# Kernel tuning notes

Hardware: AMD Instinct MI355X
Metric: run time of the kernel (lower is better)

The kernel has to match this reference:

```python
import jax, jax.numpy as jnp
import numpy as np

B, E, H, DEPTH = 4096, 512, 512, 1
STRIDE = 2 * H * (DEPTH + 1)      # 2048
DEPTH_SIZE = 2 * 4 * H            # 4096


def setup_inputs() -> dict:
    key = jax.random.key(0)
    ks = jax.random.split(key, 12)
    s = 0.02
    return {
        "X": jax.random.normal(ks[0], (B, E), jnp.float32),
        "prev_a": jax.random.normal(ks[1], (B, DEPTH + 1, H), jnp.float32),
        "prev_b": jax.random.normal(ks[2], (B, DEPTH + 1, H), jnp.float32),
        "prev_depth": jax.random.randint(ks[3], (B, 1), 0, DEPTH + 1, jnp.int32),
        "Wa00": jax.random.normal(ks[4], (H, E + 2 * H), jnp.float32) * s,
        "Wa10": jax.random.normal(ks[5], (H, E + H), jnp.float32) * s,
        "Wb00": jax.random.normal(ks[6], (H, E + 2 * H), jnp.float32) * s,
        "Wb11": jax.random.normal(ks[7], (H, E + H), jnp.float32) * s,
        "Wb10": jax.random.normal(ks[8], (H, E + H), jnp.float32) * s,
        "Wb01": jax.random.normal(ks[9], (H, E + 2 * H), jnp.float32) * s,
        "Watt": jax.random.normal(ks[10], (4, DEPTH_SIZE * DEPTH), jnp.float32) * s,
    }


def reference(X, prev_a, prev_b, prev_depth, Wa00, Wa10, Wb00, Wb11, Wb10, Wb01, Watt):
    b = X.shape[0]
    pd = prev_depth.astype(X.dtype)  # [B,1], broadcasts over feature dim
    zeros2h = jnp.zeros((b, 2 * H), X.dtype)
    ab00, ab01, ab10, ab11 = [zeros2h], [zeros2h], [zeros2h], [zeros2h]
    for d in range(1, DEPTH + 1):
        fd = jnp.float32(d)
        a_d, a_dm1 = prev_a[:, d, :], prev_a[:, d - 1, :]
        b_d, b_dm1 = prev_b[:, d, :], prev_b[:, d - 1, :]
        # 'lt' branch multiplies zeros -> drop it; keep eq/gt terms only
        eq0, gt0 = (pd == fd).astype(X.dtype), (pd > fd).astype(X.dtype)
        eqp, gtp = (pd + 1 == fd).astype(X.dtype), (pd + 1 > fd).astype(X.dtype)
        eqm, gtm = (pd - 1 == fd).astype(X.dtype), (pd - 1 > fd).astype(X.dtype)
        fork_join_a = a_d
        nofork_nojoin_a = jnp.concatenate((X, b_dm1, a_d), 1) @ Wa00.T
        fork_nojoin_a = jnp.concatenate((X, b_dm1), 1) @ Wa10.T
        nofork_join_a = a_dm1
        na00 = eq0 * nofork_nojoin_a + gt0 * a_d
        na11 = eq0 * fork_join_a + gt0 * a_d
        na10 = eqp * fork_nojoin_a + gtp * a_d
        na01 = eqm * nofork_join_a + gtm * a_d
        fork_join_b = jnp.concatenate((X, b_d), 1) @ Wb11.T
        nofork_nojoin_b = jnp.concatenate((X, a_d, na00), 1) @ Wb00.T
        fork_nojoin_b = jnp.concatenate((X, na10), 1) @ Wb10.T
        nofork_join_b = jnp.concatenate((X, b_dm1, a_d), 1) @ Wb01.T
        nb00 = eq0 * nofork_nojoin_b + gt0 * b_d
        nb11 = eq0 * fork_join_b + gt0 * b_d
        nb10 = eqp * fork_nojoin_b + gtp * b_d
        nb01 = eqm * nofork_join_b + gtm * b_d
        ab00.append(jnp.concatenate((na00, nb00), 1))
        ab01.append(jnp.concatenate((na01, nb01), 1))
        ab10.append(jnp.concatenate((na10, nb10), 1))
        ab11.append(jnp.concatenate((na11, nb11), 1))
    # each branch: stack over depth+1 -> [B, stride]; concat branches -> [B, 4*stride]
    flats = [jnp.stack(lst, 1).reshape(b, -1) for lst in (ab00, ab01, ab10, ab11)]
    ns = jnp.concatenate(flats, 1)  # [B, 4*STRIDE]
    att = jax.nn.softmax(ns[:, DEPTH_SIZE:] @ Watt.T, axis=-1)  # [B,4]
    e0 = (pd == 0).astype(X.dtype)
    ed = (pd == DEPTH).astype(X.dtype)
    mask = jnp.concatenate((1 - e0, 1 - e0, 1 - ed, 1 - e0), 1)  # [B,4]
    att_vars = mask * att
    # np tiny underflows to 0 in fp32 -> selection is one-hot at the row max
    sel = jnp.sign(att_vars - att_vars.max(1, keepdims=True)) + 1.0
    # striper/stripe_expander bmm == per-row selection of one stride-block
    hidden = jnp.einsum('bc,bcs->bs', sel, ns.reshape(b, 4, STRIDE))
    hidden = hidden.reshape(b, DEPTH + 1, 2 * H)
    next_a = hidden[:, :, :H]
    next_b = hidden[:, :, H:]
    sel_i = sel.astype(prev_depth.dtype)
    pd0 = prev_depth[:, 0]
    next_depth = (sel_i[:, 0] * pd0 + sel_i[:, 1] * (pd0 - 1)
                  + sel_i[:, 2] * (pd0 + 1) + sel_i[:, 3] * pd0)[:, None]
    f = (sel[:, 2] + sel[:, 3])[:, None]
    j = (sel[:, 1] + sel[:, 3])[:, None]
    return next_a, next_b, next_depth, (f, j)
```

## Files before the change

kernel.cpp:

```cpp
#include <hip/hip_runtime.h>
#include <hip/hip_bf16.h>
#include <stdint.h>


typedef __attribute__((ext_vector_type(8))) short bf16x8;
typedef __attribute__((ext_vector_type(4))) float f32x4;

#define MB_ ((size_t)1 << 20)

static __device__ __forceinline__ unsigned short f2bf(float x) {
  unsigned u = __float_as_uint(x);
  return (unsigned short)((u + 0x7FFFu + ((u >> 16) & 1u)) >> 16);
}
static __device__ __forceinline__ float bf2f(unsigned short b) {
  return __uint_as_float((unsigned)b << 16);
}
static __device__ __forceinline__ void cvt8(float4 v0, float4 v1, uint4& hi, uint4& lo) {
  float v[8] = {v0.x, v0.y, v0.z, v0.w, v1.x, v1.y, v1.z, v1.w};
  unsigned hw[4], lw[4];
#pragma unroll
  for (int j = 0; j < 4; ++j) {
    unsigned short h0 = f2bf(v[2 * j]), h1 = f2bf(v[2 * j + 1]);
    unsigned short l0 = f2bf(v[2 * j] - bf2f(h0));
    unsigned short l1 = f2bf(v[2 * j + 1] - bf2f(h1));
    hw[j] = (unsigned)h0 | ((unsigned)h1 << 16);
    lw[j] = (unsigned)l0 | ((unsigned)l1 << 16);
  }
  hi = make_uint4(hw[0], hw[1], hw[2], hw[3]);
  lo = make_uint4(lw[0], lw[1], lw[2], lw[3]);
}

__global__ void kinit(float* nextA, float* nextB, int* cnt, int Bn) {
  long i = (long)blockIdx.x * blockDim.x + threadIdx.x;
  long st = (long)gridDim.x * blockDim.x;
  long n4 = (long)Bn * 128;
  float4 z = make_float4(0.f, 0.f, 0.f, 0.f);
  for (long t = i; t < n4; t += st) {
    long row = t >> 7;
    int off = (int)(t & 127);
    ((float4*)(nextA + row * 1024))[off] = z;
    ((float4*)(nextB + row * 1024))[off] = z;
  }
  if (blockIdx.x == 0 && threadIdx.x < 16) cnt[threadIdx.x] = 0;
}

struct CvtSeg { const float* src; unsigned short* dst; int srcStride; int gprow; long gbase; };
struct CvtArgs { CvtSeg s[5]; long total; };

__global__ void kcvt(CvtArgs a) {
  long g0 = (long)blockIdx.x * blockDim.x + threadIdx.x;
  long st = (long)gridDim.x * blockDim.x;
  for (long g = g0; g < a.total; g += st) {
    const float* src = a.s[0].src;
    unsigned short* dst = a.s[0].dst;
    int stride = a.s[0].srcStride, gp = a.s[0].gprow;
    long base = 0;
#pragma unroll
    for (int t = 1; t < 5; ++t) {
      if (g >= a.s[t].gbase) {
        src = a.s[t].src; dst = a.s[t].dst;
        stride = a.s[t].srcStride; gp = a.s[t].gprow; base = a.s[t].gbase;
      }
    }
    long lg = g - base;
    int row = (int)(lg / gp);
    int kp = (int)(lg - (long)row * gp);
    const float* p = src + (long)row * stride + kp * 8;
    uint4 hi, lo;
    cvt8(*(const float4*)p, *(const float4*)(p + 4), hi, lo);
    unsigned short* d = dst + (long)row * ((long)gp * 16) + (long)(kp >> 2) * 64 + (kp & 3) * 8;
    *(uint4*)d = hi;
    *(uint4*)(d + 32) = lo;
  }
}

__global__ void kclassify(const int* __restrict__ pdep, float* dep, float* fo, float* jo,
                          int* cnt, int* list0, int* list1, int Bn) {
  int r = blockIdx.x * blockDim.x + threadIdx.x;
  if (r >= Bn) return;
  if (pdep[r] == 0) {
    int p = atomicAdd(&cnt[0], 1);
    list0[p] = r;
    dep[r] = 1.0f; fo[r] = 1.0f; jo[r] = 0.0f;
  } else {
    int p = atomicAdd(&cnt[1], 1);
    list1[p] = r;
  }
}

struct GArgs {
  const float *X, *pa, *pb;
  float *nb11ws, *na00ws, *na10ws;
  const unsigned short *Wa10p, *Wb10p, *Wb11p, *Wa00p, *Wb00p;
  float *nextA, *nextB;
  const int *cnt, *list0, *list1, *list2, *list2i;
};

__global__ __launch_bounds__(256, 4) void gemm_mfma(GArgs G, int modeBase, int bpm) {
  int mode = (int)blockIdx.x / bpm + modeBase;
  int bl = (int)blockIdx.x % bpm;
  int xcd = bl & 7, g = bl >> 3;
  int nt = g & 7, mt = (g >> 3) * 8 + xcd;

  const int* lst; int cntv, ksteps;
  const unsigned short* W;
  if (mode == 0)      { lst = G.list0; cntv = G.cnt[0]; ksteps = 32; W = G.Wa10p; }
  else if (mode == 1) { lst = G.list1; cntv = G.cnt[1]; ksteps = 32; W = G.Wb11p; }
  else if (mode == 2) { lst = G.list1; cntv = G.cnt[1]; ksteps = 48; W = G.Wa00p; }
  else if (mode == 3) { lst = G.list0; cntv = G.cnt[0]; ksteps = 32; W = G.Wb10p; }
  else                { lst = G.list2; cntv = G.cnt[2]; ksteps = 48; W = G.Wb00p; }
  if (mt * 64 >= cntv) return;

  const int tid = threadIdx.x;
  const int arow = tid >> 2, kg = tid & 3;
  int mg = mt * 64 + arow;
  if (mg > cntv - 1) mg = cntv - 1;
  int r01 = lst[mg];
  const float* ab0 = G.X + (long)r01 * 512 + kg * 8;
  const float* ab1;
  const float* ab2 = nullptr;
  if (mode == 0)      ab1 = G.pb + (long)r01 * 1024 + kg * 8;
  else if (mode == 1) ab1 = G.pb + (long)r01 * 1024 + 512 + kg * 8;
  else if (mode == 2) {
    ab1 = G.pb + (long)r01 * 1024 + kg * 8;
    ab2 = G.pa + (long)r01 * 1024 + 512 + kg * 8;
  } else if (mode == 3) {
    ab1 = G.na10ws + (long)mg * 512 + kg * 8;
  } else {
    ab1 = G.pa + (long)r01 * 1024 + 512 + kg * 8;
    ab2 = G.na00ws + (long)G.list2i[mg] * 512 + kg * 8;
  }
  long wb = (long)(nt * 64 + arow) * (long)(ksteps * 64) + kg * 8;

  __shared__ unsigned short lds[2][2][4096];

  float4 av0, av1;
  uint4 bhr, blr;
  auto gload = [&](int kb) {
    const float* p = (kb < 16) ? ab0 : (kb < 32) ? ab1 : ab2;
    p += (kb & 15) * 32;
    av0 = *(const float4*)p;
    av1 = *(const float4*)(p + 4);
    const unsigned short* q = W + wb + (long)kb * 64;
    bhr = *(const uint4*)q;
    blr = *(const uint4*)(q + 32);
  };
  auto lstore = [&](int b) {
    uint4 hi, lo;
    cvt8(av0, av1, hi, lo);
    *(uint4*)&lds[b][0][((kg) * 64 + arow) * 8] = hi;
    *(uint4*)&lds[b][0][((kg + 4) * 64 + arow) * 8] = lo;
    *(uint4*)&lds[b][1][((kg) * 64 + arow) * 8] = bhr;
    *(uint4*)&lds[b][1][((kg + 4) * 64 + arow) * 8] = blr;
  };

  const int w = tid >> 6, lane = tid & 63;
  const int wrow = (w >> 1) * 32, wcol = (w & 1) * 32;
  const int gq = lane >> 4, lr = lane & 15;

  f32x4 acc[2][2];
#pragma unroll
  for (int i = 0; i < 2; ++i)
#pragma unroll
    for (int j = 0; j < 2; ++j) acc[i][j] = (f32x4){0.f, 0.f, 0.f, 0.f};

  gload(0);
  lstore(0);
  __syncthreads();
  int cur = 0;
  for (int kb = 0; kb < ksteps; ++kb) {
    bf16x8 ah[2], al[2], bh[2], bl[2];
#pragma unroll
    for (int t = 0; t < 2; ++t) {
      ah[t] = *(const bf16x8*)&lds[cur][0][(gq * 64 + wrow + t * 16 + lr) * 8];
      al[t] = *(const bf16x8*)&lds[cur][0][((gq + 4) * 64 + wrow + t * 16 + lr) * 8];
      bh[t] = *(const bf16x8*)&lds[cur][1][(gq * 64 + wcol + t * 16 + lr) * 8];
      bl[t] = *(const bf16x8*)&lds[cur][1][((gq + 4) * 64 + wcol + t * 16 + lr) * 8];
    }
    if (kb + 1 < ksteps) gload(kb + 1);
#pragma unroll
    for (int rb = 0; rb < 2; ++rb)
#pragma unroll
      for (int cb = 0; cb < 2; ++cb) {
        acc[rb][cb] = __builtin_amdgcn_mfma_f32_16x16x32_bf16(ah[rb], bh[cb], acc[rb][cb], 0, 0, 0);
        acc[rb][cb] = __builtin_amdgcn_mfma_f32_16x16x32_bf16(ah[rb], bl[cb], acc[rb][cb], 0, 0, 0);
        acc[rb][cb] = __builtin_amdgcn_mfma_f32_16x16x32_bf16(al[rb], bh[cb], acc[rb][cb], 0, 0, 0);
      }
    if (kb + 1 < ksteps) lstore(cur ^ 1);
    __syncthreads();
    cur ^= 1;
  }

#pragma unroll
  for (int rb = 0; rb < 2; ++rb)
#pragma unroll
    for (int e = 0; e < 4; ++e) {
      int m = wrow + rb * 16 + (lane >> 4) * 4 + e;
      int mgo = mt * 64 + m;
      if (mgo >= cntv) continue;
#pragma unroll
      for (int cb = 0; cb < 2; ++cb) {
        int n = nt * 64 + wcol + cb * 16 + lr;
        float v = acc[rb][cb][e];
        if (mode == 0) {
          G.nextA[(long)G.list0[mgo] * 1024 + 512 + n] = v;
          G.na10ws[(long)mgo * 512 + n] = v;
        } else if (mode == 1) {
          G.nb11ws[(long)mgo * 512 + n] = v;
        } else if (mode == 2) {
          G.na00ws[(long)mgo * 512 + n] = v;
        } else if (mode == 3) {
          G.nextB[(long)G.list0[mgo] * 1024 + 512 + n] = v;
        } else {
          atomicAdd(G.nextB + (long)G.list2[mgo] * 1024 + 512 + n, v);
        }
      }
    }
}

__global__ __launch_bounds__(256) void kselect(
    const float* __restrict__ pa, const float* __restrict__ pb,
    const float* __restrict__ watt, const float* __restrict__ nb11ws,
    const float* __restrict__ na00ws,
    float* nextA, float* nextB, float* dep, float* fo, float* jo,
    int* cnt, const int* __restrict__ list1, int* list2, int* list2i) {
  int warp = threadIdx.x >> 6, lane = threadIdx.x & 63;
  int i1 = blockIdx.x * 4 + warp;
  if (i1 >= cnt[1]) return;
  int r = list1[i1];
  const float* a_d = pa + (long)r * 1024 + 512;
  const float* b_d = pb + (long)r * 1024 + 512;
  const float* nb = nb11ws + (long)i1 * 512;
  const float* na = na00ws + (long)i1 * 512;
  float av[8], nv[8];
  float z0 = 0.f, z1 = 0.f, z2 = 0.f, z3 = 0.f;
#pragma unroll
  for (int u = 0; u < 8; ++u) {
    int h = u * 64 + lane;
    float la = a_d[h], lb = b_d[h], ln = nb[h];
    av[u] = la; nv[u] = ln;
    z0 += (watt[1024 + h] + watt[3072 + h]) * la + watt[1536 + h] * lb + watt[3584 + h] * ln;
    z1 += (watt[5120 + h] + watt[7168 + h]) * la + watt[5632 + h] * lb + watt[7680 + h] * ln;
    z2 += (watt[9216 + h] + watt[11264 + h]) * la + watt[9728 + h] * lb + watt[11776 + h] * ln;
    z3 += (watt[13312 + h] + watt[15360 + h]) * la + watt[13824 + h] * lb + watt[15872 + h] * ln;
  }
#pragma unroll
  for (int off = 32; off; off >>= 1) {
    z0 += __shfl_xor(z0, off); z1 += __shfl_xor(z1, off);
    z2 += __shfl_xor(z2, off); z3 += __shfl_xor(z3, off);
  }
  float m = fmaxf(fmaxf(z0, z1), fmaxf(z2, z3));
  float e0 = expf(z0 - m), e1 = expf(z1 - m), e2 = expf(z2 - m), e3 = expf(z3 - m);
  float s = e0 + e1 + e2 + e3;
  float att0 = e0 / s, att1 = e1 / s, att3 = e3 / s;
  float amax = fmaxf(att0, fmaxf(att1, att3));
  float s0 = (att0 >= amax) ? 1.f : 0.f;
  float s1v = (att1 >= amax) ? 1.f : 0.f;
  float s3 = (att3 >= amax) ? 1.f : 0.f;
  if (lane == 0) {
    dep[r] = s0 + s3;
    fo[r] = s3;
    jo[r] = s1v + s3;
    if (s0 > 0.f) { int p = atomicAdd(&cnt[2], 1); list2[p] = r; list2i[p] = i1; }
  }
  float* dA = nextA + (long)r * 1024 + 512;
  float* dB = nextB + (long)r * 1024 + 512;
#pragma unroll
  for (int u = 0; u < 8; ++u) {
    int h = u * 64 + lane;
    float va = s3 * av[u];
    if (s0 > 0.f) va += na[h];
    dA[h] = va;
    dB[h] = s3 * nv[u];
  }
}

extern "C" void kernel_launch(void* const* d_in, const int* in_sizes, int n_in,
                              void* d_out, int out_size, void* d_ws, size_t ws_size,
                              hipStream_t stream) {
  const float* X = (const float*)d_in[0];
  const float* pa = (const float*)d_in[1];
  const float* pb = (const float*)d_in[2];
  const int* pdep = (const int*)d_in[3];
  const float* Wa00 = (const float*)d_in[4];
  const float* Wa10 = (const float*)d_in[5];
  const float* Wb00 = (const float*)d_in[6];
  const float* Wb11 = (const float*)d_in[7];
  const float* Wb10 = (const float*)d_in[8];
  const float* Watt = (const float*)d_in[10];
  const int Bn = in_sizes[3];

  float* out = (float*)d_out;
  float* nextA = out;
  float* nextB = out + (long)Bn * 1024;
  float* dep = out + (long)2 * Bn * 1024;
  float* fo = dep + Bn;
  float* jo = fo + Bn;

  char* ws = (char*)d_ws;
  int* cnt = (int*)ws;
  int* list0 = (int*)(ws + 1024);
  int* list1 = (int*)(ws + 1024 + 16384);
  int* list2 = (int*)(ws + 1024 + 2 * 16384);
  int* list2i = (int*)(ws + 1024 + 3 * 16384);
  float* nb11ws = (float*)(ws + 1 * MB_);
  float* na00ws = (float*)(ws + 9 * MB_);
  float* na10ws = (float*)(ws + 17 * MB_);
  unsigned short* Wa10p = (unsigned short*)(ws + 25 * MB_);
  unsigned short* Wb10p = (unsigned short*)(ws + 27 * MB_);
  unsigned short* Wb11p = (unsigned short*)(ws + 29 * MB_);
  unsigned short* Wa00p = (unsigned short*)(ws + 31 * MB_);
  unsigned short* Wb00p = (unsigned short*)(ws + 34 * MB_);

  kinit<<<1024, 256, 0, stream>>>(nextA, nextB, cnt, Bn);

  CvtArgs ca{};
  long gb = 0;
  auto seg = [&](int i, const float* s, unsigned short* d, int stride, int gprow, int rows) {
    ca.s[i].src = s; ca.s[i].dst = d; ca.s[i].srcStride = stride;
    ca.s[i].gprow = gprow; ca.s[i].gbase = gb;
    gb += (long)gprow * rows;
  };
  seg(0, Wa10, Wa10p, 1024, 128, 512);
  seg(1, Wb10, Wb10p, 1024, 128, 512);
  seg(2, Wb11, Wb11p, 1024, 128, 512);
  seg(3, Wa00, Wa00p, 1536, 192, 512);
  seg(4, Wb00, Wb00p, 1536, 192, 512);
  ca.total = gb;
  kcvt<<<512, 256, 0, stream>>>(ca);

  kclassify<<<(Bn + 255) / 256, 256, 0, stream>>>(pdep, dep, fo, jo, cnt, list0, list1, Bn);

  GArgs Ga;
  Ga.X = X; Ga.pa = pa; Ga.pb = pb;
  Ga.nb11ws = nb11ws; Ga.na00ws = na00ws; Ga.na10ws = na10ws;
  Ga.Wa10p = Wa10p; Ga.Wb10p = Wb10p; Ga.Wb11p = Wb11p;
  Ga.Wa00p = Wa00p; Ga.Wb00p = Wb00p;
  Ga.nextA = nextA; Ga.nextB = nextB;
  Ga.cnt = cnt; Ga.list0 = list0; Ga.list1 = list1; Ga.list2 = list2; Ga.list2i = list2i;

  int nmb = (Bn + 63) / 64;
  int nm8 = ((nmb + 7) / 8) * 8;
  int bpm = nm8 * 8;

  gemm_mfma<<<3 * bpm, 256, 0, stream>>>(Ga, 0, bpm);
  kselect<<<(Bn + 3) / 4, 256, 0, stream>>>(pa, pb, Watt, nb11ws, na00ws, nextA, nextB,
                                            dep, fo, jo, cnt, list1, list2, list2i);
  gemm_mfma<<<bpm, 256, 0, stream>>>(Ga, 3, bpm);
  gemm_mfma<<<bpm, 256, 0, stream>>>(Ga, 4, bpm);
}
```

Baseline: 265.8 us.

## Split-K later GEMMs with atomics, drop lo-A MFMA term, swizzle LDS

Modes 3 and 4 now run split-K across 16-step chunks (2 and 3 groups), accumulating into nextB with atomicAdd. kinit therefore zeros all of nextB. All modes except mode 1 drop the A-low bf16 correction term, which cuts MFMAs per step from 3 to 2 and removes one LDS store and read. LDS indexing gets an XOR swizzle to reduce bank conflicts, and the next global load is issued before the LDS reads. Risks are lower precision from the dropped split-bf16 term and more atomic traffic.

```diff
diff --git a/kernel.cpp b/kernel.cpp
--- a/kernel.cpp
+++ b/kernel.cpp
@@ -33,14 +33,12 @@
 __global__ void kinit(float* nextA, float* nextB, int* cnt, int Bn) {
   long i = (long)blockIdx.x * blockDim.x + threadIdx.x;
   long st = (long)gridDim.x * blockDim.x;
-  long n4 = (long)Bn * 128;
   float4 z = make_float4(0.f, 0.f, 0.f, 0.f);
-  for (long t = i; t < n4; t += st) {
-    long row = t >> 7;
-    int off = (int)(t & 127);
-    ((float4*)(nextA + row * 1024))[off] = z;
-    ((float4*)(nextB + row * 1024))[off] = z;
-  }
+  long nA = (long)Bn * 128;
+  for (long t = i; t < nA; t += st)
+    ((float4*)(nextA + (t >> 7) * 1024))[t & 127] = z;
+  long nB = (long)Bn * 256;
+  for (long t = i; t < nB; t += st) ((float4*)nextB)[t] = z;
   if (blockIdx.x == 0 && threadIdx.x < 16) cnt[threadIdx.x] = 0;
 }
 
@@ -97,19 +95,25 @@
 };
 
 __global__ __launch_bounds__(256, 4) void gemm_mfma(GArgs G, int modeBase, int bpm) {
-  int mode = (int)blockIdx.x / bpm + modeBase;
+  int grp = (int)blockIdx.x / bpm;
   int bl = (int)blockIdx.x % bpm;
+  int mode, ks;
+  if (modeBase == 0) { mode = grp; ks = 0; }
+  else { mode = modeBase; ks = grp; }
   int xcd = bl & 7, g = bl >> 3;
   int nt = g & 7, mt = (g >> 3) * 8 + xcd;
 
-  const int* lst; int cntv, ksteps;
+  const int* lst; int cntv, ktot;
   const unsigned short* W;
-  if (mode == 0)      { lst = G.list0; cntv = G.cnt[0]; ksteps = 32; W = G.Wa10p; }
-  else if (mode == 1) { lst = G.list1; cntv = G.cnt[1]; ksteps = 32; W = G.Wb11p; }
-  else if (mode == 2) { lst = G.list1; cntv = G.cnt[1]; ksteps = 48; W = G.Wa00p; }
-  else if (mode == 3) { lst = G.list0; cntv = G.cnt[0]; ksteps = 32; W = G.Wb10p; }
-  else                { lst = G.list2; cntv = G.cnt[2]; ksteps = 48; W = G.Wb00p; }
+  if (mode == 0)      { lst = G.list0; cntv = G.cnt[0]; ktot = 32; W = G.Wa10p; }
+  else if (mode == 1) { lst = G.list1; cntv = G.cnt[1]; ktot = 32; W = G.Wb11p; }
+  else if (mode == 2) { lst = G.list1; cntv = G.cnt[1]; ktot = 48; W = G.Wa00p; }
+  else if (mode == 3) { lst = G.list0; cntv = G.cnt[0]; ktot = 32; W = G.Wb10p; }
+  else                { lst = G.list2; cntv = G.cnt[2]; ktot = 48; W = G.Wb00p; }
   if (mt * 64 >= cntv) return;
+  const bool full3 = (mode == 1);
+  const int kb0 = ks * 16;
+  const int kb1 = (modeBase == 0) ? ktot : kb0 + 16;
 
   const int tid = threadIdx.x;
   const int arow = tid >> 2, kg = tid & 3;
@@ -130,7 +134,7 @@
     ab1 = G.pa + (long)r01 * 1024 + 512 + kg * 8;
     ab2 = G.na00ws + (long)G.list2i[mg] * 512 + kg * 8;
   }
-  long wb = (long)(nt * 64 + arow) * (long)(ksteps * 64) + kg * 8;
+  long wb = (long)(nt * 64 + arow) * (long)(ktot * 64) + kg * 8;
 
   __shared__ unsigned short lds[2][2][4096];
 
@@ -148,10 +152,11 @@
   auto lstore = [&](int b) {
     uint4 hi, lo;
     cvt8(av0, av1, hi, lo);
-    *(uint4*)&lds[b][0][((kg) * 64 + arow) * 8] = hi;
-    *(uint4*)&lds[b][0][((kg + 4) * 64 + arow) * 8] = lo;
-    *(uint4*)&lds[b][1][((kg) * 64 + arow) * 8] = bhr;
-    *(uint4*)&lds[b][1][((kg + 4) * 64 + arow) * 8] = blr;
+    *(uint4*)&lds[b][0][(kg * 64 + (arow ^ kg)) * 8] = hi;
+    if (full3)
+      *(uint4*)&lds[b][0][((kg + 4) * 64 + (arow ^ (kg + 4))) * 8] = lo;
+    *(uint4*)&lds[b][1][(kg * 64 + (arow ^ kg)) * 8] = bhr;
+    *(uint4*)&lds[b][1][((kg + 4) * 64 + (arow ^ (kg + 4))) * 8] = blr;
   };
 
   const int w = tid >> 6, lane = tid & 63;
@@ -164,29 +169,32 @@
 #pragma unroll
     for (int j = 0; j < 2; ++j) acc[i][j] = (f32x4){0.f, 0.f, 0.f, 0.f};
 
-  gload(0);
+  gload(kb0);
   lstore(0);
   __syncthreads();
   int cur = 0;
-  for (int kb = 0; kb < ksteps; ++kb) {
+  for (int kb = kb0; kb < kb1; ++kb) {
+    if (kb + 1 < kb1) gload(kb + 1);
     bf16x8 ah[2], al[2], bh[2], bl[2];
 #pragma unroll
     for (int t = 0; t < 2; ++t) {
-      ah[t] = *(const bf16x8*)&lds[cur][0][(gq * 64 + wrow + t * 16 + lr) * 8];
-      al[t] = *(const bf16x8*)&lds[cur][0][((gq + 4) * 64 + wrow + t * 16 + lr) * 8];
-      bh[t] = *(const bf16x8*)&lds[cur][1][(gq * 64 + wcol + t * 16 + lr) * 8];
-      bl[t] = *(const bf16x8*)&lds[cur][1][((gq + 4) * 64 + wcol + t * 16 + lr) * 8];
+      int rr = wrow + t * 16 + lr, cc = wcol + t * 16 + lr;
+      ah[t] = *(const bf16x8*)&lds[cur][0][(gq * 64 + (rr ^ gq)) * 8];
+      bh[t] = *(const bf16x8*)&lds[cur][1][(gq * 64 + (cc ^ gq)) * 8];
+      bl[t] = *(const bf16x8*)&lds[cur][1][((gq + 4) * 64 + (cc ^ (gq + 4))) * 8];
+      if (full3)
+        al[t] = *(const bf16x8*)&lds[cur][0][((gq + 4) * 64 + (rr ^ (gq + 4))) * 8];
     }
-    if (kb + 1 < ksteps) gload(kb + 1);
 #pragma unroll
     for (int rb = 0; rb < 2; ++rb)
 #pragma unroll
       for (int cb = 0; cb < 2; ++cb) {
         acc[rb][cb] = __builtin_amdgcn_mfma_f32_16x16x32_bf16(ah[rb], bh[cb], acc[rb][cb], 0, 0, 0);
         acc[rb][cb] = __builtin_amdgcn_mfma_f32_16x16x32_bf16(ah[rb], bl[cb], acc[rb][cb], 0, 0, 0);
-        acc[rb][cb] = __builtin_amdgcn_mfma_f32_16x16x32_bf16(al[rb], bh[cb], acc[rb][cb], 0, 0, 0);
+        if (full3)
+          acc[rb][cb] = __builtin_amdgcn_mfma_f32_16x16x32_bf16(al[rb], bh[cb], acc[rb][cb], 0, 0, 0);
       }
-    if (kb + 1 < ksteps) lstore(cur ^ 1);
+    if (kb + 1 < kb1) lstore(cur ^ 1);
     __syncthreads();
     cur ^= 1;
   }
@@ -209,10 +217,8 @@
           G.nb11ws[(long)mgo * 512 + n] = v;
         } else if (mode == 2) {
           G.na00ws[(long)mgo * 512 + n] = v;
-        } else if (mode == 3) {
-          G.nextB[(long)G.list0[mgo] * 1024 + 512 + n] = v;
         } else {
-          atomicAdd(G.nextB + (long)G.list2[mgo] * 1024 + 512 + n, v);
+          atomicAdd(G.nextB + (long)lst[mgo] * 1024 + 512 + n, v);
         }
       }
     }
@@ -346,6 +352,6 @@
   gemm_mfma<<<3 * bpm, 256, 0, stream>>>(Ga, 0, bpm);
   kselect<<<(Bn + 3) / 4, 256, 0, stream>>>(pa, pb, Watt, nb11ws, na00ws, nextA, nextB,
                                             dep, fo, jo, cnt, list1, list2, list2i);
-  gemm_mfma<<<bpm, 256, 0, stream>>>(Ga, 3, bpm);
-  gemm_mfma<<<bpm, 256, 0, stream>>>(Ga, 4, bpm);
-}
+  gemm_mfma<<<2 * bpm, 256, 0, stream>>>(Ga, 3, bpm);
+  gemm_mfma<<<3 * bpm, 256, 0, stream>>>(Ga, 4, bpm);
+}
```

Result: faster. 236.9 us (-10.9%).
